# Performance work log

Measured on AMD Instinct MI355X. Metric: run time of the kernel, lower is better.

Reference implementation:

```python
import jax, jax.numpy as jnp
from jax import lax
import numpy as np

B, T, D = 8, 2048, 1024


def setup_inputs() -> dict:
    key = jax.random.key(0)
    ks = jax.random.split(key, 10)
    s = 1.0 / np.sqrt(D)
    return {
        "x": jax.random.normal(ks[0], (B, T, D), jnp.float32),
        "last_x": jax.random.normal(ks[1], (B, D), jnp.float32),
        "aa": jnp.zeros((B, D), jnp.float32),
        "bb": jnp.zeros((B, D), jnp.float32),
        "pp": jnp.zeros((B, D), jnp.float32),
        "time_mix_k": jax.random.uniform(ks[2], (1, 1, D), jnp.float32),
        "time_mix_v": jax.random.uniform(ks[3], (1, 1, D), jnp.float32),
        "time_mix_r": jax.random.uniform(ks[4], (1, 1, D), jnp.float32),
        "time_first": jax.random.normal(ks[5], (1, D), jnp.float32) * 0.5,
        "time_decay": -jnp.abs(jax.random.normal(ks[6], (1, D), jnp.float32)),
        "Wk": jax.random.normal(ks[7], (D, D), jnp.float32) * s,
        "Wv": jax.random.normal(ks[8], (D, D), jnp.float32) * s,
        "Wr": jax.random.normal(ks[9], (D, D), jnp.float32) * s,
        "Wo": jax.random.normal(jax.random.fold_in(key, 99), (D, D), jnp.float32) * s,
    }


def _wkv_scan(k, v, aa, bb, pp, time_first, time_decay):
    # k, v: [B, T, D]; carries aa/bb/pp: [B, D]
    def step(carry, kv):
        aa, bb, pp = carry
        kt, vt = kv  # [B, D]
        ww = time_first + kt
        qq = jnp.maximum(pp, ww)
        e1 = jnp.exp(pp - qq)
        e2 = jnp.exp(ww - qq)
        wkv = (e1 * aa + e2 * vt) / (e1 * bb + e2)
        ww2 = pp + time_decay
        qq2 = jnp.maximum(ww2, kt)
        e1b = jnp.exp(ww2 - qq2)
        e2b = jnp.exp(kt - qq2)
        return (e1b * aa + e2b * vt, e1b * bb + e2b, qq2), wkv

    (aa, bb, pp), wkv = lax.scan(
        step, (aa, bb, pp), (k.swapaxes(0, 1), v.swapaxes(0, 1))
    )
    return wkv.swapaxes(0, 1), aa, bb, pp


def reference(x, last_x, aa, bb, pp, time_mix_k, time_mix_v, time_mix_r,
              time_first, time_decay, Wk, Wv, Wr, Wo):
    # xx = token-shifted x with last_x prepended
    xx = jnp.concatenate([last_x[:, None, :], x[:, :-1, :]], axis=1)
    xk = x * time_mix_k + xx * (1.0 - time_mix_k)
    xv = x * time_mix_v + xx * (1.0 - time_mix_v)
    xr = x * time_mix_r + xx * (1.0 - time_mix_r)
    r = jax.nn.sigmoid(jnp.einsum('btd,de->bte', xr, Wr))
    k = jnp.einsum('btd,de->bte', xk, Wk)
    v = jnp.einsum('btd,de->bte', xv, Wv)
    wkv, new_aa, new_bb, new_pp = _wkv_scan(k, v, aa, bb, pp, time_first, time_decay)
    out = jnp.einsum('btd,de->bte', r * wkv, Wo)
    return out, x[:, -1, :], new_aa, new_bb, new_pp
```

## Files before the change

### kernel.cpp

```cpp
#include <hip/hip_runtime.h>
#include <hip/hip_bf16.h>
#include <stdint.h>

#define D_DIM 1024
#define B_DIM 8
#define T_DIM 2048
#define M_DIM (B_DIM * T_DIM)
#define CHUNK 32
#define NCHUNK (T_DIM / CHUNK)
#define NCH (B_DIM * D_DIM)

typedef __attribute__((ext_vector_type(8))) short bf16x8;
typedef __attribute__((ext_vector_type(4))) float f32x4;

__device__ __forceinline__ unsigned short f2bf(float f) {
    union { float f; uint32_t u; } c; c.f = f;
    uint32_t u = c.u;
    u += 0x7fffu + ((u >> 16) & 1u);
    return (unsigned short)(u >> 16);
}
__device__ __forceinline__ float bf2f(unsigned short h) {
    union { uint32_t u; float f; } c; c.u = ((uint32_t)h) << 16;
    return c.f;
}

__global__ void transpose_to_bf16(const float* __restrict__ W,
                                  unsigned short* __restrict__ WT) {
    __shared__ float tile[32][33];
    int tx = threadIdx.x, ty = threadIdx.y;
    int x0 = blockIdx.x * 32, y0 = blockIdx.y * 32;
#pragma unroll
    for (int i = 0; i < 4; i++) {
        int r = ty + i * 8;
        tile[r][tx] = W[(size_t)(y0 + r) * D_DIM + x0 + tx];
    }
    __syncthreads();
#pragma unroll
    for (int i = 0; i < 4; i++) {
        int r = ty + i * 8;
        WT[(size_t)(x0 + r) * D_DIM + y0 + tx] = f2bf(tile[tx][r]);
    }
}

__global__ void lerp_kernel(const float* __restrict__ x,
                            const float* __restrict__ last_x,
                            const float* __restrict__ tmk,
                            const float* __restrict__ tmv,
                            const float* __restrict__ tmr,
                            unsigned short* __restrict__ xk,
                            unsigned short* __restrict__ xv,
                            unsigned short* __restrict__ xr) {
    int gid = blockIdx.x * blockDim.x + threadIdx.x;
    size_t e = (size_t)gid * 4;
    int m = (int)(e >> 10);
    int c = (int)(e & 1023);
    int t = m & (T_DIM - 1);
    int b = m >> 11;
    float4 xc = *(const float4*)(x + e);
    float4 xp;
    if (t == 0) xp = *(const float4*)(last_x + (size_t)b * D_DIM + c);
    else        xp = *(const float4*)(x + e - D_DIM);
    float4 mk = *(const float4*)(tmk + c);
    float4 mv = *(const float4*)(tmv + c);
    float4 mr = *(const float4*)(tmr + c);

    ushort4 ok, ov, orr;
    ok.x = f2bf(xp.x + mk.x * (xc.x - xp.x));
    ok.y = f2bf(xp.y + mk.y * (xc.y - xp.y));
    ok.z = f2bf(xp.z + mk.z * (xc.z - xp.z));
    ok.w = f2bf(xp.w + mk.w * (xc.w - xp.w));
    ov.x = f2bf(xp.x + mv.x * (xc.x - xp.x));
    ov.y = f2bf(xp.y + mv.y * (xc.y - xp.y));
    ov.z = f2bf(xp.z + mv.z * (xc.z - xp.z));
    ov.w = f2bf(xp.w + mv.w * (xc.w - xp.w));
    orr.x = f2bf(xp.x + mr.x * (xc.x - xp.x));
    orr.y = f2bf(xp.y + mr.y * (xc.y - xp.y));
    orr.z = f2bf(xp.z + mr.z * (xc.z - xp.z));
    orr.w = f2bf(xp.w + mr.w * (xc.w - xp.w));
    *(ushort4*)(xk + e) = ok;
    *(ushort4*)(xv + e) = ov;
    *(ushort4*)(xr + e) = orr;
}

template <int MODE>
__global__ __launch_bounds__(256) void gemm_bf16(
    const unsigned short* __restrict__ A,
    const unsigned short* __restrict__ BT,
    void* __restrict__ Cout) {
    __shared__ __align__(16) unsigned short As[128 * 40];
    __shared__ __align__(16) unsigned short Bs[128 * 40];
    int tid = threadIdx.x;
    int wave = tid >> 6, lane = tid & 63;
    int wr = wave >> 1, wc = wave & 1;
    int l16 = lane & 15, q = lane >> 4;
    int m0 = blockIdx.y * 128, n0 = blockIdx.x * 128;

    f32x4 acc[4][4] = {};

    for (int k0 = 0; k0 < D_DIM; k0 += 32) {
#pragma unroll
        for (int i = 0; i < 2; i++) {
            int eidx = (i * 256 + tid) * 8;
            int r = eidx >> 5, c = eidx & 31;
            *(uint4*)(&As[r * 40 + c]) =
                *(const uint4*)(A + (size_t)(m0 + r) * D_DIM + k0 + c);
            *(uint4*)(&Bs[r * 40 + c]) =
                *(const uint4*)(BT + (size_t)(n0 + r) * D_DIM + k0 + c);
        }
        __syncthreads();

        bf16x8 af[4], bfr[4];
#pragma unroll
        for (int mi = 0; mi < 4; mi++)
            af[mi] = *(const bf16x8*)(&As[(wr * 64 + mi * 16 + l16) * 40 + q * 8]);
#pragma unroll
        for (int ni = 0; ni < 4; ni++)
            bfr[ni] = *(const bf16x8*)(&Bs[(wc * 64 + ni * 16 + l16) * 40 + q * 8]);
#pragma unroll
        for (int mi = 0; mi < 4; mi++)
#pragma unroll
            for (int ni = 0; ni < 4; ni++)
                acc[mi][ni] = __builtin_amdgcn_mfma_f32_16x16x32_bf16(
                    af[mi], bfr[ni], acc[mi][ni], 0, 0, 0);
        __syncthreads();
    }

#pragma unroll
    for (int mi = 0; mi < 4; mi++) {
#pragma unroll
        for (int ni = 0; ni < 4; ni++) {
#pragma unroll
            for (int reg = 0; reg < 4; reg++) {
                int row = m0 + wr * 64 + mi * 16 + q * 4 + reg;
                int col = n0 + wc * 64 + ni * 16 + l16;
                float val = acc[mi][ni][reg];
                if (MODE == 1) val = 1.0f / (1.0f + __expf(-val));
                if (MODE == 2)
                    ((float*)Cout)[(size_t)row * D_DIM + col] = val;
                else
                    ((unsigned short*)Cout)[(size_t)row * D_DIM + col] = f2bf(val);
            }
        }
    }
}

__global__ void wkv_phase1(const unsigned short* __restrict__ kbuf,
                           const unsigned short* __restrict__ vbuf,
                           const float* __restrict__ td_arr,
                           float* __restrict__ laa,
                           float* __restrict__ lbb,
                           float* __restrict__ lpp) {
    int g = blockIdx.x * blockDim.x + threadIdx.x;
    int ch = g & (NCH - 1);
    int c = g >> 13;
    int d = ch & (D_DIM - 1);
    int b = ch >> 10;
    float td = td_arr[d];
    float aa = 0.f, bb = 0.f, pp = -1e30f;
    size_t base = (size_t)b * T_DIM * D_DIM + (size_t)(c * CHUNK) * D_DIM + d;
    for (int t = 0; t < CHUNK; t++) {
        size_t idx = base + (size_t)t * D_DIM;
        float kt = bf2f(kbuf[idx]);
        float vt = bf2f(vbuf[idx]);
        float ww2 = pp + td;
        float qq2 = fmaxf(ww2, kt);
        float e1b = __expf(ww2 - qq2);
        float e2b = __expf(kt - qq2);
        aa = e1b * aa + e2b * vt;
        bb = e1b * bb + e2b;
        pp = qq2;
    }
    laa[g] = aa;
    lbb[g] = bb;
    lpp[g] = pp;
}

__global__ void wkv_phase2(const float* __restrict__ aa_in,
                           const float* __restrict__ bb_in,
                           const float* __restrict__ pp_in,
                           const float* __restrict__ td_arr,
                           const float* __restrict__ x,
                           float* __restrict__ laa,
                           float* __restrict__ lbb,
                           float* __restrict__ lpp,
                           float* __restrict__ lastx_out,
                           float* __restrict__ aa_out,
                           float* __restrict__ bb_out,
                           float* __restrict__ pp_out) {
    int ch = blockIdx.x * blockDim.x + threadIdx.x;
    int d = ch & (D_DIM - 1);
    int b = ch >> 10;
    float td = td_arr[d];
    float Ldecay = (float)CHUNK * td;
    float A = aa_in[ch], Bv = bb_in[ch], P = pp_in[ch];
    for (int c = 0; c < NCHUNK; c++) {
        int idx = c * NCH + ch;
        float la = laa[idx], lb = lbb[idx], lp = lpp[idx];
        laa[idx] = A; lbb[idx] = Bv; lpp[idx] = P;
        float Pd = P + Ldecay;
        float q = fmaxf(Pd, lp);
        float e1 = __expf(Pd - q);
        float e2 = __expf(lp - q);
        A = e1 * A + e2 * la;
        Bv = e1 * Bv + e2 * lb;
        P = q;
    }
    aa_out[ch] = A;
    bb_out[ch] = Bv;
    pp_out[ch] = P;
    lastx_out[ch] =
        x[(size_t)b * T_DIM * D_DIM + (size_t)(T_DIM - 1) * D_DIM + d];
}

__global__ void wkv_phase3(const unsigned short* __restrict__ kbuf,
                           const unsigned short* __restrict__ vbuf,
                           const unsigned short* __restrict__ rbuf,
                           const float* __restrict__ tf_arr,
                           const float* __restrict__ td_arr,
                           const float* __restrict__ laa,
                           const float* __restrict__ lbb,
                           const float* __restrict__ lpp,
                           unsigned short* __restrict__ rwkv) {
    int g = blockIdx.x * blockDim.x + threadIdx.x;
    int ch = g & (NCH - 1);
    int c = g >> 13;
    int d = ch & (D_DIM - 1);
    int b = ch >> 10;
    float tf = tf_arr[d], td = td_arr[d];
    float aa = laa[g], bb = lbb[g], pp = lpp[g];
    size_t base = (size_t)b * T_DIM * D_DIM + (size_t)(c * CHUNK) * D_DIM + d;
    for (int t = 0; t < CHUNK; t++) {
        size_t idx = base + (size_t)t * D_DIM;
        float kt = bf2f(kbuf[idx]);
        float vt = bf2f(vbuf[idx]);
        float rt = bf2f(rbuf[idx]);
        float ww = tf + kt;
        float qq = fmaxf(pp, ww);
        float e1 = __expf(pp - qq);
        float e2 = __expf(ww - qq);
        float wkv = (e1 * aa + e2 * vt) / (e1 * bb + e2);
        rwkv[idx] = f2bf(rt * wkv);
        float ww2 = pp + td;
        float qq2 = fmaxf(ww2, kt);
        float e1b = __expf(ww2 - qq2);
        float e2b = __expf(kt - qq2);
        aa = e1b * aa + e2b * vt;
        bb = e1b * bb + e2b;
        pp = qq2;
    }
}

extern "C" void kernel_launch(void* const* d_in, const int* in_sizes, int n_in,
                              void* d_out, int out_size, void* d_ws,
                              size_t ws_size, hipStream_t stream) {
    const float* x      = (const float*)d_in[0];
    const float* last_x = (const float*)d_in[1];
    const float* aa     = (const float*)d_in[2];
    const float* bb     = (const float*)d_in[3];
    const float* pp     = (const float*)d_in[4];
    const float* tmk    = (const float*)d_in[5];
    const float* tmv    = (const float*)d_in[6];
    const float* tmr    = (const float*)d_in[7];
    const float* tf     = (const float*)d_in[8];
    const float* td     = (const float*)d_in[9];
    const float* Wk     = (const float*)d_in[10];
    const float* Wv     = (const float*)d_in[11];
    const float* Wr     = (const float*)d_in[12];
    const float* Wo     = (const float*)d_in[13];

    unsigned short* WkT = (unsigned short*)d_ws;
    unsigned short* WvT = WkT + (size_t)D_DIM * D_DIM;
    unsigned short* WrT = WvT + (size_t)D_DIM * D_DIM;
    unsigned short* WoT = WrT + (size_t)D_DIM * D_DIM;
    unsigned short* xk  = WoT + (size_t)D_DIM * D_DIM;
    unsigned short* xv  = xk + (size_t)M_DIM * D_DIM;
    unsigned short* xr  = xv + (size_t)M_DIM * D_DIM;
    unsigned short* kb  = xr + (size_t)M_DIM * D_DIM;
    unsigned short* vb   = xk;
    unsigned short* rb   = xv;
    unsigned short* rwkv = xr;

    float* laa = (float*)WkT;
    float* lbb = (float*)WvT;
    float* lpp = (float*)WrT;

    float* out       = (float*)d_out;
    float* lastx_out = out + (size_t)M_DIM * D_DIM;
    float* aa_out    = lastx_out + B_DIM * D_DIM;
    float* bb_out    = aa_out + B_DIM * D_DIM;
    float* pp_out    = bb_out + B_DIM * D_DIM;

    dim3 tb(32, 8), tg(32, 32);
    transpose_to_bf16<<<tg, tb, 0, stream>>>(Wk, WkT);
    transpose_to_bf16<<<tg, tb, 0, stream>>>(Wv, WvT);
    transpose_to_bf16<<<tg, tb, 0, stream>>>(Wr, WrT);
    transpose_to_bf16<<<tg, tb, 0, stream>>>(Wo, WoT);

    lerp_kernel<<<(M_DIM * D_DIM / 4) / 256, 256, 0, stream>>>(
        x, last_x, tmk, tmv, tmr, xk, xv, xr);

    dim3 gg(D_DIM / 128, M_DIM / 128);
    gemm_bf16<0><<<gg, 256, 0, stream>>>(xk, WkT, kb);
    gemm_bf16<0><<<gg, 256, 0, stream>>>(xv, WvT, vb);
    gemm_bf16<1><<<gg, 256, 0, stream>>>(xr, WrT, rb);

    wkv_phase1<<<(NCH * NCHUNK) / 256, 256, 0, stream>>>(kb, vb, td, laa, lbb, lpp);
    wkv_phase2<<<NCH / 256, 256, 0, stream>>>(aa, bb, pp, td, x, laa, lbb, lpp,
                                              lastx_out, aa_out, bb_out, pp_out);
    wkv_phase3<<<(NCH * NCHUNK) / 256, 256, 0, stream>>>(
        kb, vb, rb, tf, td, laa, lbb, lpp, rwkv);

    gemm_bf16<2><<<gg, 256, 0, stream>>>(rwkv, WoT, out);
}
```

Before: 462.6 us.

## Load GEMM tiles directly into LDS and batch weight transposes in one launch

The GEMM kernel now uses global_load_lds to move A and B tiles straight from global memory into shared memory, skipping the register round trip. The LDS padding is dropped so each wave's 16-row chunk is laid out contiguously as the instruction requires. The grid is reordered so blocks iterate over M first, and the four weight transposes are merged into a single launch via blockIdx.z. The unpadded layout may introduce LDS bank conflicts on the fragment reads.

```diff
diff --git a/kernel.cpp b/kernel.cpp
--- a/kernel.cpp
+++ b/kernel.cpp
@@ -24,8 +24,25 @@
     return c.f;
 }
 
-__global__ void transpose_to_bf16(const float* __restrict__ W,
-                                  unsigned short* __restrict__ WT) {
+__device__ __forceinline__ void gload_lds16(const unsigned short* g,
+                                            unsigned short* lds_base) {
+    __builtin_amdgcn_global_load_lds(
+        (const __attribute__((address_space(1))) unsigned int*)g,
+        (__attribute__((address_space(3))) unsigned int*)lds_base, 16, 0, 0);
+}
+
+__global__ void transpose_to_bf16(const float* __restrict__ W0,
+                                  const float* __restrict__ W1,
+                                  const float* __restrict__ W2,
+                                  const float* __restrict__ W3,
+                                  unsigned short* __restrict__ WT0,
+                                  unsigned short* __restrict__ WT1,
+                                  unsigned short* __restrict__ WT2,
+                                  unsigned short* __restrict__ WT3) {
+    const float* W = (blockIdx.z == 0) ? W0 : (blockIdx.z == 1) ? W1
+                     : (blockIdx.z == 2) ? W2 : W3;
+    unsigned short* WT = (blockIdx.z == 0) ? WT0 : (blockIdx.z == 1) ? WT1
+                         : (blockIdx.z == 2) ? WT2 : WT3;
     __shared__ float tile[32][33];
     int tx = threadIdx.x, ty = threadIdx.y;
     int x0 = blockIdx.x * 32, y0 = blockIdx.y * 32;
@@ -87,35 +104,41 @@
     const unsigned short* __restrict__ A,
     const unsigned short* __restrict__ BT,
     void* __restrict__ Cout) {
-    __shared__ __align__(16) unsigned short As[128 * 40];
-    __shared__ __align__(16) unsigned short Bs[128 * 40];
+    __shared__ __align__(16) unsigned short As[128 * 32];
+    __shared__ __align__(16) unsigned short Bs[128 * 32];
     int tid = threadIdx.x;
     int wave = tid >> 6, lane = tid & 63;
     int wr = wave >> 1, wc = wave & 1;
     int l16 = lane & 15, q = lane >> 4;
-    int m0 = blockIdx.y * 128, n0 = blockIdx.x * 128;
+    int m0 = blockIdx.x * 128, n0 = blockIdx.y * 128;
+
+    int r0 = tid >> 2, c0 = (tid & 3) * 8;
+    int r1 = 64 + r0, c1 = c0;
+    unsigned short* lA0 = &As[wave * 512];
+    unsigned short* lA1 = &As[2048 + wave * 512];
+    unsigned short* lB0 = &Bs[wave * 512];
+    unsigned short* lB1 = &Bs[2048 + wave * 512];
+    const unsigned short* gA0 = A + (size_t)(m0 + r0) * D_DIM + c0;
+    const unsigned short* gA1 = A + (size_t)(m0 + r1) * D_DIM + c1;
+    const unsigned short* gB0 = BT + (size_t)(n0 + r0) * D_DIM + c0;
+    const unsigned short* gB1 = BT + (size_t)(n0 + r1) * D_DIM + c1;
 
     f32x4 acc[4][4] = {};
 
     for (int k0 = 0; k0 < D_DIM; k0 += 32) {
-#pragma unroll
-        for (int i = 0; i < 2; i++) {
-            int eidx = (i * 256 + tid) * 8;
-            int r = eidx >> 5, c = eidx & 31;
-            *(uint4*)(&As[r * 40 + c]) =
-                *(const uint4*)(A + (size_t)(m0 + r) * D_DIM + k0 + c);
-            *(uint4*)(&Bs[r * 40 + c]) =
-                *(const uint4*)(BT + (size_t)(n0 + r) * D_DIM + k0 + c);
-        }
+        gload_lds16(gA0 + k0, lA0);
+        gload_lds16(gA1 + k0, lA1);
+        gload_lds16(gB0 + k0, lB0);
+        gload_lds16(gB1 + k0, lB1);
         __syncthreads();
 
         bf16x8 af[4], bfr[4];
 #pragma unroll
         for (int mi = 0; mi < 4; mi++)
-            af[mi] = *(const bf16x8*)(&As[(wr * 64 + mi * 16 + l16) * 40 + q * 8]);
+            af[mi] = *(const bf16x8*)(&As[(wr * 64 + mi * 16 + l16) * 32 + q * 8]);
 #pragma unroll
         for (int ni = 0; ni < 4; ni++)
-            bfr[ni] = *(const bf16x8*)(&Bs[(wc * 64 + ni * 16 + l16) * 40 + q * 8]);
+            bfr[ni] = *(const bf16x8*)(&Bs[(wc * 64 + ni * 16 + l16) * 32 + q * 8]);
 #pragma unroll
         for (int mi = 0; mi < 4; mi++)
 #pragma unroll
@@ -290,16 +313,13 @@
     float* bb_out    = aa_out + B_DIM * D_DIM;
     float* pp_out    = bb_out + B_DIM * D_DIM;
 
-    dim3 tb(32, 8), tg(32, 32);
-    transpose_to_bf16<<<tg, tb, 0, stream>>>(Wk, WkT);
-    transpose_to_bf16<<<tg, tb, 0, stream>>>(Wv, WvT);
-    transpose_to_bf16<<<tg, tb, 0, stream>>>(Wr, WrT);
-    transpose_to_bf16<<<tg, tb, 0, stream>>>(Wo, WoT);
+    dim3 tb(32, 8), tg(32, 32, 4);
+    transpose_to_bf16<<<tg, tb, 0, stream>>>(Wk, Wv, Wr, Wo, WkT, WvT, WrT, WoT);
 
     lerp_kernel<<<(M_DIM * D_DIM / 4) / 256, 256, 0, stream>>>(
         x, last_x, tmk, tmv, tmr, xk, xv, xr);
 
-    dim3 gg(D_DIM / 128, M_DIM / 128);
+    dim3 gg(M_DIM / 128, D_DIM / 128);
     gemm_bf16<0><<<gg, 256, 0, stream>>>(xk, WkT, kb);
     gemm_bf16<0><<<gg, 256, 0, stream>>>(xv, WvT, vb);
     gemm_bf16<1><<<gg, 256, 0, stream>>>(xr, WrT, rb);
```

Measured after the change: 417.9 us. 1.11x faster.

## Fold time-mix into weights and fuse K/V/R projections into one double-buffered GEMM

Applied to the files above, without the earlier changes.

Folds the time-mix lerp into the weights, so xk/xv/xr become one GEMM over [x, shifted x] with K=2048 and N=3072. It also replaces the separate lerp kernel and three GEMM launches with a bf16 cast of x plus one fused GEMM. The GEMMs now use double-buffered direct global-to-LDS loads, and k/v are stored interleaved in the output buffer as scratch. This removes three intermediate activation arrays and extra launches, but doubles the MFMA work for the projections and drops LDS padding, which may add bank conflicts.

```diff
diff --git a/kernel.cpp b/kernel.cpp
--- a/kernel.cpp
+++ b/kernel.cpp
@@ -10,22 +10,37 @@
 #define NCHUNK (T_DIM / CHUNK)
 #define NCH (B_DIM * D_DIM)
 
+typedef unsigned short us;
 typedef __attribute__((ext_vector_type(8))) short bf16x8;
 typedef __attribute__((ext_vector_type(4))) float f32x4;
 
-__device__ __forceinline__ unsigned short f2bf(float f) {
+__device__ __forceinline__ us f2bf(float f) {
     union { float f; uint32_t u; } c; c.f = f;
     uint32_t u = c.u;
     u += 0x7fffu + ((u >> 16) & 1u);
-    return (unsigned short)(u >> 16);
-}
-__device__ __forceinline__ float bf2f(unsigned short h) {
+    return (us)(u >> 16);
+}
+__device__ __forceinline__ float bf2f(us h) {
     union { uint32_t u; float f; } c; c.u = ((uint32_t)h) << 16;
     return c.f;
 }
 
-__global__ void transpose_to_bf16(const float* __restrict__ W,
-                                  unsigned short* __restrict__ WT) {
+__device__ __forceinline__ void gload_lds16(const us* g, us* lds_base) {
+    __builtin_amdgcn_global_load_lds(
+        (const __attribute__((address_space(1))) unsigned int*)g,
+        (__attribute__((address_space(3))) unsigned int*)lds_base, 16, 0, 0);
+}
+
+__global__ void prep_weights(const float* __restrict__ Wk,
+                             const float* __restrict__ Wv,
+                             const float* __restrict__ Wr,
+                             const float* __restrict__ tmk,
+                             const float* __restrict__ tmv,
+                             const float* __restrict__ tmr,
+                             us* __restrict__ WfT) {
+    int g = blockIdx.z;
+    const float* W = (g == 0) ? Wk : (g == 1) ? Wv : Wr;
+    const float* mix = (g == 0) ? tmk : (g == 1) ? tmv : tmr;
     __shared__ float tile[32][33];
     int tx = threadIdx.x, ty = threadIdx.y;
     int x0 = blockIdx.x * 32, y0 = blockIdx.y * 32;
@@ -35,6 +50,29 @@
         tile[r][tx] = W[(size_t)(y0 + r) * D_DIM + x0 + tx];
     }
     __syncthreads();
+    float mx = mix[y0 + tx];
+#pragma unroll
+    for (int i = 0; i < 4; i++) {
+        int r = ty + i * 8;
+        int n = g * 1024 + x0 + r;
+        int d = y0 + tx;
+        float w = tile[tx][r];
+        WfT[(size_t)n * 2048 + d] = f2bf(w * mx);
+        WfT[(size_t)n * 2048 + 1024 + d] = f2bf(w * (1.0f - mx));
+    }
+}
+
+__global__ void transpose_wo(const float* __restrict__ W,
+                             us* __restrict__ WT) {
+    __shared__ float tile[32][33];
+    int tx = threadIdx.x, ty = threadIdx.y;
+    int x0 = blockIdx.x * 32, y0 = blockIdx.y * 32;
+#pragma unroll
+    for (int i = 0; i < 4; i++) {
+        int r = ty + i * 8;
+        tile[r][tx] = W[(size_t)(y0 + r) * D_DIM + x0 + tx];
+    }
+    __syncthreads();
 #pragma unroll
     for (int i = 0; i < 4; i++) {
         int r = ty + i * 8;
@@ -42,89 +80,82 @@
     }
 }
 
-__global__ void lerp_kernel(const float* __restrict__ x,
-                            const float* __restrict__ last_x,
-                            const float* __restrict__ tmk,
-                            const float* __restrict__ tmv,
-                            const float* __restrict__ tmr,
-                            unsigned short* __restrict__ xk,
-                            unsigned short* __restrict__ xv,
-                            unsigned short* __restrict__ xr) {
-    int gid = blockIdx.x * blockDim.x + threadIdx.x;
-    size_t e = (size_t)gid * 4;
-    int m = (int)(e >> 10);
-    int c = (int)(e & 1023);
-    int t = m & (T_DIM - 1);
-    int b = m >> 11;
-    float4 xc = *(const float4*)(x + e);
-    float4 xp;
-    if (t == 0) xp = *(const float4*)(last_x + (size_t)b * D_DIM + c);
-    else        xp = *(const float4*)(x + e - D_DIM);
-    float4 mk = *(const float4*)(tmk + c);
-    float4 mv = *(const float4*)(tmv + c);
-    float4 mr = *(const float4*)(tmr + c);
-
-    ushort4 ok, ov, orr;
-    ok.x = f2bf(xp.x + mk.x * (xc.x - xp.x));
-    ok.y = f2bf(xp.y + mk.y * (xc.y - xp.y));
-    ok.z = f2bf(xp.z + mk.z * (xc.z - xp.z));
-    ok.w = f2bf(xp.w + mk.w * (xc.w - xp.w));
-    ov.x = f2bf(xp.x + mv.x * (xc.x - xp.x));
-    ov.y = f2bf(xp.y + mv.y * (xc.y - xp.y));
-    ov.z = f2bf(xp.z + mv.z * (xc.z - xp.z));
-    ov.w = f2bf(xp.w + mv.w * (xc.w - xp.w));
-    orr.x = f2bf(xp.x + mr.x * (xc.x - xp.x));
-    orr.y = f2bf(xp.y + mr.y * (xc.y - xp.y));
-    orr.z = f2bf(xp.z + mr.z * (xc.z - xp.z));
-    orr.w = f2bf(xp.w + mr.w * (xc.w - xp.w));
-    *(ushort4*)(xk + e) = ok;
-    *(ushort4*)(xv + e) = ov;
-    *(ushort4*)(xr + e) = orr;
-}
-
-template <int MODE>
-__global__ __launch_bounds__(256) void gemm_bf16(
-    const unsigned short* __restrict__ A,
-    const unsigned short* __restrict__ BT,
-    void* __restrict__ Cout) {
-    __shared__ __align__(16) unsigned short As[128 * 40];
-    __shared__ __align__(16) unsigned short Bs[128 * 40];
+__global__ void cast_x(const float* __restrict__ x,
+                       const float* __restrict__ last_x,
+                       us* __restrict__ xall) {
+    int row = blockIdx.x;
+    int b = row / (T_DIM + 1);
+    int t = row - b * (T_DIM + 1);
+    const float* src = (t == 0) ? (last_x + (size_t)b * D_DIM)
+                                : (x + ((size_t)b * T_DIM + t - 1) * D_DIM);
+    int c = threadIdx.x * 4;
+    float4 v = *(const float4*)(src + c);
+    ushort4 o;
+    o.x = f2bf(v.x); o.y = f2bf(v.y); o.z = f2bf(v.z); o.w = f2bf(v.w);
+    *(ushort4*)(xall + (size_t)row * D_DIM + c) = o;
+}
+
+__global__ __launch_bounds__(256) void gemm_fused(
+    const us* __restrict__ xall,
+    const us* __restrict__ WfT,
+    us* __restrict__ kvout,
+    us* __restrict__ rout) {
+    __shared__ __align__(16) us As[2][128 * 32];
+    __shared__ __align__(16) us Bs[2][128 * 32];
     int tid = threadIdx.x;
     int wave = tid >> 6, lane = tid & 63;
     int wr = wave >> 1, wc = wave & 1;
     int l16 = lane & 15, q = lane >> 4;
-    int m0 = blockIdx.y * 128, n0 = blockIdx.x * 128;
+    int m0 = blockIdx.x * 128, n0 = blockIdx.y * 128;
+    int b = m0 >> 11;
+
+    int r0 = tid >> 2, c0 = (tid & 3) * 8;
+    us* lA0 = &As[0][wave * 512];
+    us* lA1 = &As[0][2048 + wave * 512];
+    us* lB0 = &Bs[0][wave * 512];
+    us* lB1 = &Bs[0][2048 + wave * 512];
+    const us* gA1_0 = xall + (size_t)(m0 + b + 1 + r0) * 1024 + c0;
+    const us* gA1_1 = xall + (size_t)(m0 + b + 1 + 64 + r0) * 1024 + c0;
+    const us* gA2_0 = xall + (size_t)(m0 + b + r0) * 1024 + c0 - 1024;
+    const us* gA2_1 = xall + (size_t)(m0 + b + 64 + r0) * 1024 + c0 - 1024;
+    const us* gB0 = WfT + (size_t)(n0 + r0) * 2048 + c0;
+    const us* gB1 = WfT + (size_t)(n0 + 64 + r0) * 2048 + c0;
 
     f32x4 acc[4][4] = {};
 
-    for (int k0 = 0; k0 < D_DIM; k0 += 32) {
-#pragma unroll
-        for (int i = 0; i < 2; i++) {
-            int eidx = (i * 256 + tid) * 8;
-            int r = eidx >> 5, c = eidx & 31;
-            *(uint4*)(&As[r * 40 + c]) =
-                *(const uint4*)(A + (size_t)(m0 + r) * D_DIM + k0 + c);
-            *(uint4*)(&Bs[r * 40 + c]) =
-                *(const uint4*)(BT + (size_t)(n0 + r) * D_DIM + k0 + c);
+    gload_lds16(gA1_0, lA0);
+    gload_lds16(gA1_1, lA1);
+    gload_lds16(gB0, lB0);
+    gload_lds16(gB1, lB1);
+
+    for (int k0 = 0; k0 < 2048; k0 += 32) {
+        int cur = (k0 >> 5) & 1, nxt = cur ^ 1;
+        __syncthreads();
+        int kn = k0 + 32;
+        if (kn < 2048) {
+            const us* a0 = (kn < 1024) ? gA1_0 : gA2_0;
+            const us* a1 = (kn < 1024) ? gA1_1 : gA2_1;
+            gload_lds16(a0 + kn, &As[nxt][wave * 512]);
+            gload_lds16(a1 + kn, &As[nxt][2048 + wave * 512]);
+            gload_lds16(gB0 + kn, &Bs[nxt][wave * 512]);
+            gload_lds16(gB1 + kn, &Bs[nxt][2048 + wave * 512]);
         }
-        __syncthreads();
-
         bf16x8 af[4], bfr[4];
 #pragma unroll
         for (int mi = 0; mi < 4; mi++)
-            af[mi] = *(const bf16x8*)(&As[(wr * 64 + mi * 16 + l16) * 40 + q * 8]);
+            af[mi] = *(const bf16x8*)(&As[cur][(wr * 64 + mi * 16 + l16) * 32 + q * 8]);
 #pragma unroll
         for (int ni = 0; ni < 4; ni++)
-            bfr[ni] = *(const bf16x8*)(&Bs[(wc * 64 + ni * 16 + l16) * 40 + q * 8]);
+            bfr[ni] = *(const bf16x8*)(&Bs[cur][(wc * 64 + ni * 16 + l16) * 32 + q * 8]);
 #pragma unroll
         for (int mi = 0; mi < 4; mi++)
 #pragma unroll
             for (int ni = 0; ni < 4; ni++)
                 acc[mi][ni] = __builtin_amdgcn_mfma_f32_16x16x32_bf16(
                     af[mi], bfr[ni], acc[mi][ni], 0, 0, 0);
-        __syncthreads();
-    }
-
+    }
+
+    int grp = n0 >> 10;
 #pragma unroll
     for (int mi = 0; mi < 4; mi++) {
 #pragma unroll
@@ -134,18 +165,80 @@
                 int row = m0 + wr * 64 + mi * 16 + q * 4 + reg;
                 int col = n0 + wc * 64 + ni * 16 + l16;
                 float val = acc[mi][ni][reg];
-                if (MODE == 1) val = 1.0f / (1.0f + __expf(-val));
-                if (MODE == 2)
-                    ((float*)Cout)[(size_t)row * D_DIM + col] = val;
-                else
-                    ((unsigned short*)Cout)[(size_t)row * D_DIM + col] = f2bf(val);
+                if (grp < 2) {
+                    kvout[(size_t)row * 2048 + col] = f2bf(val);
+                } else {
+                    val = 1.0f / (1.0f + __expf(-val));
+                    rout[(size_t)row * 1024 + (col - 2048)] = f2bf(val);
+                }
             }
         }
     }
 }
 
-__global__ void wkv_phase1(const unsigned short* __restrict__ kbuf,
-                           const unsigned short* __restrict__ vbuf,
+__global__ __launch_bounds__(256) void gemm_out(
+    const us* __restrict__ A,
+    const us* __restrict__ BT,
+    float* __restrict__ Cout) {
+    __shared__ __align__(16) us As[2][128 * 32];
+    __shared__ __align__(16) us Bs[2][128 * 32];
+    int tid = threadIdx.x;
+    int wave = tid >> 6, lane = tid & 63;
+    int wr = wave >> 1, wc = wave & 1;
+    int l16 = lane & 15, q = lane >> 4;
+    int m0 = blockIdx.x * 128, n0 = blockIdx.y * 128;
+
+    int r0 = tid >> 2, c0 = (tid & 3) * 8;
+    const us* gA0 = A + (size_t)(m0 + r0) * 1024 + c0;
+    const us* gA1 = A + (size_t)(m0 + 64 + r0) * 1024 + c0;
+    const us* gB0 = BT + (size_t)(n0 + r0) * 1024 + c0;
+    const us* gB1 = BT + (size_t)(n0 + 64 + r0) * 1024 + c0;
+
+    f32x4 acc[4][4] = {};
+
+    gload_lds16(gA0, &As[0][wave * 512]);
+    gload_lds16(gA1, &As[0][2048 + wave * 512]);
+    gload_lds16(gB0, &Bs[0][wave * 512]);
+    gload_lds16(gB1, &Bs[0][2048 + wave * 512]);
+
+    for (int k0 = 0; k0 < 1024; k0 += 32) {
+        int cur = (k0 >> 5) & 1, nxt = cur ^ 1;
+        __syncthreads();
+        int kn = k0 + 32;
+        if (kn < 1024) {
+            gload_lds16(gA0 + kn, &As[nxt][wave * 512]);
+            gload_lds16(gA1 + kn, &As[nxt][2048 + wave * 512]);
+            gload_lds16(gB0 + kn, &Bs[nxt][wave * 512]);
+            gload_lds16(gB1 + kn, &Bs[nxt][2048 + wave * 512]);
+        }
+        bf16x8 af[4], bfr[4];
+#pragma unroll
+        for (int mi = 0; mi < 4; mi++)
+            af[mi] = *(const bf16x8*)(&As[cur][(wr * 64 + mi * 16 + l16) * 32 + q * 8]);
+#pragma unroll
+        for (int ni = 0; ni < 4; ni++)
+            bfr[ni] = *(const bf16x8*)(&Bs[cur][(wc * 64 + ni * 16 + l16) * 32 + q * 8]);
+#pragma unroll
+        for (int mi = 0; mi < 4; mi++)
+#pragma unroll
+            for (int ni = 0; ni < 4; ni++)
+                acc[mi][ni] = __builtin_amdgcn_mfma_f32_16x16x32_bf16(
+                    af[mi], bfr[ni], acc[mi][ni], 0, 0, 0);
+    }
+
+#pragma unroll
+    for (int mi = 0; mi < 4; mi++)
+#pragma unroll
+        for (int ni = 0; ni < 4; ni++)
+#pragma unroll
+            for (int reg = 0; reg < 4; reg++) {
+                int row = m0 + wr * 64 + mi * 16 + q * 4 + reg;
+                int col = n0 + wc * 64 + ni * 16 + l16;
+                Cout[(size_t)row * 1024 + col] = acc[mi][ni][reg];
+            }
+}
+
+__global__ void wkv_phase1(const us* __restrict__ kvbuf,
                            const float* __restrict__ td_arr,
                            float* __restrict__ laa,
                            float* __restrict__ lbb,
@@ -157,11 +250,11 @@
     int b = ch >> 10;
     float td = td_arr[d];
     float aa = 0.f, bb = 0.f, pp = -1e30f;
-    size_t base = (size_t)b * T_DIM * D_DIM + (size_t)(c * CHUNK) * D_DIM + d;
+    size_t row = (size_t)b * T_DIM + (size_t)c * CHUNK;
     for (int t = 0; t < CHUNK; t++) {
-        size_t idx = base + (size_t)t * D_DIM;
-        float kt = bf2f(kbuf[idx]);
-        float vt = bf2f(vbuf[idx]);
+        size_t rbase = (row + t) * 2048;
+        float kt = bf2f(kvbuf[rbase + d]);
+        float vt = bf2f(kvbuf[rbase + 1024 + d]);
         float ww2 = pp + td;
         float qq2 = fmaxf(ww2, kt);
         float e1b = __expf(ww2 - qq2);
@@ -212,15 +305,13 @@
         x[(size_t)b * T_DIM * D_DIM + (size_t)(T_DIM - 1) * D_DIM + d];
 }
 
-__global__ void wkv_phase3(const unsigned short* __restrict__ kbuf,
-                           const unsigned short* __restrict__ vbuf,
-                           const unsigned short* __restrict__ rbuf,
+__global__ void wkv_phase3(const us* __restrict__ kvbuf,
+                           us* __restrict__ rbuf,
                            const float* __restrict__ tf_arr,
                            const float* __restrict__ td_arr,
                            const float* __restrict__ laa,
                            const float* __restrict__ lbb,
-                           const float* __restrict__ lpp,
-                           unsigned short* __restrict__ rwkv) {
+                           const float* __restrict__ lpp) {
     int g = blockIdx.x * blockDim.x + threadIdx.x;
     int ch = g & (NCH - 1);
     int c = g >> 13;
@@ -228,18 +319,19 @@
     int b = ch >> 10;
     float tf = tf_arr[d], td = td_arr[d];
     float aa = laa[g], bb = lbb[g], pp = lpp[g];
-    size_t base = (size_t)b * T_DIM * D_DIM + (size_t)(c * CHUNK) * D_DIM + d;
+    size_t row = (size_t)b * T_DIM + (size_t)c * CHUNK;
     for (int t = 0; t < CHUNK; t++) {
-        size_t idx = base + (size_t)t * D_DIM;
-        float kt = bf2f(kbuf[idx]);
-        float vt = bf2f(vbuf[idx]);
-        float rt = bf2f(rbuf[idx]);
+        size_t rbase = (row + t) * 2048;
+        size_t ridx = (row + t) * 1024 + d;
+        float kt = bf2f(kvbuf[rbase + d]);
+        float vt = bf2f(kvbuf[rbase + 1024 + d]);
+        float rt = bf2f(rbuf[ridx]);
         float ww = tf + kt;
         float qq = fmaxf(pp, ww);
         float e1 = __expf(pp - qq);
         float e2 = __expf(ww - qq);
         float wkv = (e1 * aa + e2 * vt) / (e1 * bb + e2);
-        rwkv[idx] = f2bf(rt * wkv);
+        rbuf[ridx] = f2bf(rt * wkv);
         float ww2 = pp + td;
         float qq2 = fmaxf(ww2, kt);
         float e1b = __expf(ww2 - qq2);
@@ -268,21 +360,14 @@
     const float* Wr     = (const float*)d_in[12];
     const float* Wo     = (const float*)d_in[13];
 
-    unsigned short* WkT = (unsigned short*)d_ws;
-    unsigned short* WvT = WkT + (size_t)D_DIM * D_DIM;
-    unsigned short* WrT = WvT + (size_t)D_DIM * D_DIM;
-    unsigned short* WoT = WrT + (size_t)D_DIM * D_DIM;
-    unsigned short* xk  = WoT + (size_t)D_DIM * D_DIM;
-    unsigned short* xv  = xk + (size_t)M_DIM * D_DIM;
-    unsigned short* xr  = xv + (size_t)M_DIM * D_DIM;
-    unsigned short* kb  = xr + (size_t)M_DIM * D_DIM;
-    unsigned short* vb   = xk;
-    unsigned short* rb   = xv;
-    unsigned short* rwkv = xr;
-
-    float* laa = (float*)WkT;
-    float* lbb = (float*)WvT;
-    float* lpp = (float*)WrT;
+    us* WfT  = (us*)d_ws;
+    us* WoT  = WfT + (size_t)3072 * 2048;
+    us* xall = WoT + (size_t)D_DIM * D_DIM;
+    us* rb   = xall + (size_t)B_DIM * (T_DIM + 1) * D_DIM;
+
+    float* laa = (float*)xall;
+    float* lbb = laa + (size_t)NCH * NCHUNK;
+    float* lpp = lbb + (size_t)NCH * NCHUNK;
 
     float* out       = (float*)d_out;
     float* lastx_out = out + (size_t)M_DIM * D_DIM;
@@ -290,25 +375,21 @@
     float* bb_out    = aa_out + B_DIM * D_DIM;
     float* pp_out    = bb_out + B_DIM * D_DIM;
 
-    dim3 tb(32, 8), tg(32, 32);
-    transpose_to_bf16<<<tg, tb, 0, stream>>>(Wk, WkT);
-    transpose_to_bf16<<<tg, tb, 0, stream>>>(Wv, WvT);
-    transpose_to_bf16<<<tg, tb, 0, stream>>>(Wr, WrT);
-    transpose_to_bf16<<<tg, tb, 0, stream>>>(Wo, WoT);
-
-    lerp_kernel<<<(M_DIM * D_DIM / 4) / 256, 256, 0, stream>>>(
-        x, last_x, tmk, tmv, tmr, xk, xv, xr);
-
-    dim3 gg(D_DIM / 128, M_DIM / 128);
-    gemm_bf16<0><<<gg, 256, 0, stream>>>(xk, WkT, kb);
-    gemm_bf16<0><<<gg, 256, 0, stream>>>(xv, WvT, vb);
-    gemm_bf16<1><<<gg, 256, 0, stream>>>(xr, WrT, rb);
-
-    wkv_phase1<<<(NCH * NCHUNK) / 256, 256, 0, stream>>>(kb, vb, td, laa, lbb, lpp);
+    us* kvbuf = (us*)d_out;
+
+    prep_weights<<<dim3(32, 32, 3), dim3(32, 8), 0, stream>>>(
+        Wk, Wv, Wr, tmk, tmv, tmr, WfT);
+    transpose_wo<<<dim3(32, 32), dim3(32, 8), 0, stream>>>(Wo, WoT);
+    cast_x<<<B_DIM * (T_DIM + 1), 256, 0, stream>>>(x, last_x, xall);
+
+    gemm_fused<<<dim3(M_DIM / 128, 3072 / 128), 256, 0, stream>>>(
+        xall, WfT, kvbuf, rb);
+
+    wkv_phase1<<<(NCH * NCHUNK) / 256, 256, 0, stream>>>(kvbuf, td, laa, lbb, lpp);
     wkv_phase2<<<NCH / 256, 256, 0, stream>>>(aa, bb, pp, td, x, laa, lbb, lpp,
                                               lastx_out, aa_out, bb_out, pp_out);
     wkv_phase3<<<(NCH * NCHUNK) / 256, 256, 0, stream>>>(
-        kb, vb, rb, tf, td, laa, lbb, lpp, rwkv);
-
-    gemm_bf16<2><<<gg, 256, 0, stream>>>(rwkv, WoT, out);
-}
+        kvbuf, rb, tf, td, laa, lbb, lpp);
+
+    gemm_out<<<dim3(M_DIM / 128, D_DIM / 128), 256, 0, stream>>>(rb, WoT, out);
+}
```

New measurement: 506.3 us. 9.4% more time.
